# Optimization experiments

Hardware: AMD Instinct MI355X
Metric: run time of the kernel (lower is better)

Reference implementation:

```python
import jax, jax.numpy as jnp
import numpy as np

B, LIN, LOUT = 16, 100, 100
V, D, AD, H, HID = 32000, 512, 64, 8, 2048
RECYCLE, PAD = 1, 0
SCALE = float(np.sqrt(AD))

def _pe(L, dim):
    # positional(pos, i) = pos / 10000 ** ((i//2)/dim); sin on even i, cos on odd i
    pos = jnp.arange(L, dtype=jnp.float32)[:, None]
    i = jnp.arange(dim)
    ang = pos / jnp.power(jnp.float32(10000.0), (i // 2).astype(jnp.float32) / dim)
    return jnp.where(i % 2 == 0, jnp.sin(ang), jnp.cos(ang))  # (L, dim)

def _ln(x, g, b):
    m = x.mean(-1, keepdims=True)
    v = ((x - m) ** 2).mean(-1, keepdims=True)
    return (x - m) / jnp.sqrt(v + 1e-5) * g + b

def _mha(q, k, v, mask, p):
    wq, bq, wk, bk, wv, bv, wo, bo, g, b = p
    m, lq, _ = q.shape
    lk = k.shape[1]
    Q = (q @ wq + bq).reshape(m, lq, H, AD).transpose(0, 2, 1, 3)
    K = (k @ wk + bk).reshape(m, lk, H, AD).transpose(0, 2, 1, 3)
    Vh = (v @ wv + bv).reshape(m, lk, H, AD).transpose(0, 2, 1, 3)
    attn = jnp.einsum('mnld,mnkd->mnlk', Q / SCALE, K)
    attn = jnp.where(mask[:, None, :, :], attn, jnp.float32(-1e9))
    attn = jax.nn.softmax(attn, axis=-1)
    o = jnp.einsum('mnlk,mnkd->mnld', attn, Vh)
    # original uses rearrange 'm n l d -> m l (d n)': d is the OUTER factor
    o = o.transpose(0, 2, 3, 1).reshape(m, lq, AD * H)
    o = o @ wo + bo + q  # dropout is identity in eval
    return _ln(o, g, b)

def _ff(x, w1, b1, w2, b2, g, b):
    return _ln(jax.nn.relu(x @ w1 + b1) @ w2 + b2 + x, g, b)

def _forward(floats, inputs, outputs):
    (sw, fcb,
     ewq, ebq, ewk, ebk, ewv, ebv, ewo, ebo, eg1, eb1, ef1w, ef1b, ef2w, ef2b, eg2, eb2,
     dwq, dbq, dwk, dbk, dwv, dbv, dwo, dbo, dg1, db1, df1w, df1b, df2w, df2b, dg2, db2) = floats
    enc_p = (ewq, ebq, ewk, ebk, ewv, ebv, ewo, ebo, eg1, eb1)
    dec_p = (dwq, dbq, dwk, dbk, dwv, dbv, dwo, dbo, dg1, db1)
    in_mask = (inputs != PAD)[:, None, :]                    # (B,1,LIN) -> bcast (B,1,1,LIN)
    tril = jnp.tril(jnp.ones((LOUT, LOUT), dtype=bool))
    out_mask = (outputs != PAD)[:, None, :] & tril[None]     # (B,LOUT,LOUT)
    enc = sw[inputs] + _pe(LIN, D)[None]
    for _ in range(RECYCLE + 1):  # shared weights reused each iteration
        enc = _mha(enc, enc, enc, in_mask, enc_p)
        enc = _ff(enc, ef1w, ef1b, ef2w, ef2b, eg2, eb2)
    dec = sw[outputs] + _pe(LOUT, D)[None]
    for _ in range(RECYCLE + 1):  # same MHA module for self- and cross-attention
        dec = _mha(dec, dec, dec, out_mask, dec_p)
        dec = _mha(dec, enc, enc, in_mask, dec_p)
        dec = _ff(dec, df1w, df1b, df2w, df2b, dg2, db2)
    dec = dec * jnp.float32(D ** -0.5)
    logits = dec @ sw.T + fcb  # fc.weight tied to share_weight
    return jax.nn.softmax(logits, axis=-1)

def setup_inputs():
    key = jax.random.key(0)
    ks = iter(jax.random.split(key, 64))
    rn = lambda shape: jax.random.normal(next(ks), shape, dtype=jnp.float32) * 0.02
    z = lambda shape: jnp.zeros(shape, jnp.float32)
    o = lambda shape: jnp.ones(shape, jnp.float32)
    d = {'inputs': jax.random.randint(next(ks), (B, LIN), 0, V),
         'outputs': jax.random.randint(next(ks), (B, LOUT), 0, V),
         'share_weight': rn((V, D)), 'fc_b': z((V,))}
    for p in ('enc', 'dec'):
        d[f'{p}_wq'] = rn((D, H * AD)); d[f'{p}_bq'] = z((H * AD,))
        d[f'{p}_wk'] = rn((D, H * AD)); d[f'{p}_bk'] = z((H * AD,))
        d[f'{p}_wv'] = rn((D, H * AD)); d[f'{p}_bv'] = z((H * AD,))
        d[f'{p}_wo'] = rn((H * AD, D)); d[f'{p}_bo'] = z((D,))
        d[f'{p}_g1'] = o((D,)); d[f'{p}_b1'] = z((D,))
        d[f'{p}_f1w'] = rn((D, HID)); d[f'{p}_f1b'] = z((HID,))
        d[f'{p}_f2w'] = rn((HID, D)); d[f'{p}_f2b'] = z((D,))
        d[f'{p}_g2'] = o((D,)); d[f'{p}_b2'] = z((D,))
    return d

def reference(inputs, outputs, share_weight, fc_b, enc_wq, enc_bq, enc_wk, enc_bk, enc_wv, enc_bv, enc_wo, enc_bo, enc_g1, enc_b1, enc_f1w, enc_f1b, enc_f2w, enc_f2b, enc_g2, enc_b2, dec_wq, dec_bq, dec_wk, dec_bk, dec_wv, dec_bv, dec_wo, dec_bo, dec_g1, dec_b1, dec_f1w, dec_f1b, dec_f2w, dec_f2b, dec_g2, dec_b2):
    floats = (share_weight, fc_b, enc_wq, enc_bq, enc_wk, enc_bk, enc_wv, enc_bv, enc_wo, enc_bo, enc_g1, enc_b1, enc_f1w, enc_f1b, enc_f2w, enc_f2b, enc_g2, enc_b2, dec_wq, dec_bq, dec_wk, dec_bk, dec_wv, dec_bv, dec_wo, dec_bo, dec_g1, dec_b1, dec_f1w, dec_f1b, dec_f2w, dec_f2b, dec_g2, dec_b2)
    return _forward(floats, inputs, outputs)
```

## Files before the change

kernel.cpp:

```cpp
#include <hip/hip_runtime.h>

#define TQ     1600
#define MP     1664
#define DM     512
#define NHD    8
#define HD     64
#define VOCAB  32000
#define HID    2048
#define LSEQ   100
#define NSTRIPE 500
#define SCALEV 0.044194173824159216f

typedef unsigned short u16;
typedef unsigned int u32;
typedef __attribute__((ext_vector_type(8))) short bf16x8;
typedef __attribute__((ext_vector_type(4))) float f32x4;

__device__ __forceinline__ u16 f2b(float x) {
  union { float f; unsigned u; } c; c.f = x;
  unsigned r = (c.u + 0x7FFFu + ((c.u >> 16) & 1u)) >> 16;
  return (u16)r;
}
__device__ __forceinline__ float b2f(u16 b) {
  union { unsigned u; float f; } c; c.u = ((unsigned)b) << 16; return c.f;
}
__device__ __forceinline__ unsigned pk2(float lo, float hi) {
  return (unsigned)f2b(lo) | ((unsigned)f2b(hi) << 16);
}
__device__ __forceinline__ float wredsum(float v) {
#pragma unroll
  for (int o = 32; o > 0; o >>= 1) v += __shfl_xor(v, o, 64);
  return v;
}

struct PrepArgs {
  const float* wsrc[12];
  u16* wdst[12];
  int K[12], N[12], toff[12];
  int ntile;
  const float* bsrc[6];
  float* qbE; float* qbD; float* peT;
};

__global__ __launch_bounds__(256) void prep_kernel(PrepArgs a) {
  __shared__ float t[64][65];
  int bid = blockIdx.x, tid = threadIdx.x;
  if (bid < a.ntile) {
    int wi = 0;
#pragma unroll
    for (int i = 1; i < 12; ++i) if (bid >= a.toff[i]) wi = i;
    int tile = bid - a.toff[wi];
    int K = a.K[wi], N = a.N[wi];
    int ktiles = K >> 6;
    int k0 = (tile % ktiles) << 6, n0 = (tile / ktiles) << 6;
    const float* src = a.wsrc[wi];
    u16* dst = a.wdst[wi];
    int r = tid >> 4, c = (tid & 15) * 4;
#pragma unroll
    for (int i = 0; i < 4; ++i) {
      float4 v = *(const float4*)(src + (size_t)(k0 + r + i * 16) * N + n0 + c);
      t[r + i * 16][c + 0] = v.x; t[r + i * 16][c + 1] = v.y;
      t[r + i * 16][c + 2] = v.z; t[r + i * 16][c + 3] = v.w;
    }
    __syncthreads();
#pragma unroll
    for (int i = 0; i < 4; ++i) {
      int n = r + i * 16;
      ushort4 o;
      o.x = f2b(t[c + 0][n]); o.y = f2b(t[c + 1][n]);
      o.z = f2b(t[c + 2][n]); o.w = f2b(t[c + 3][n]);
      *(ushort4*)(dst + (size_t)(n0 + n) * K + k0 + c) = o;
    }
  } else if (bid < a.ntile + 12) {
    int j = (bid - a.ntile) * 256 + tid;
    if (j < 3072) {
      int which = j >> 9, o = j & 511;
      float v = a.bsrc[which][o];
      if (which < 3) a.qbE[which * 512 + o] = v;
      else           a.qbD[(which - 3) * 512 + o] = v;
    }
  } else {
    int idx = (bid - a.ntile - 12) * 256 + tid;
    if (idx < LSEQ * 512) {
      int l = idx >> 9, d = idx & 511;
      float freq = expf(-(float)(d >> 1) * (9.210340371976184f / 512.0f));
      float ang = (float)l * freq;
      a.peT[idx] = (d & 1) ? cosf(ang) : sinf(ang);
    }
  }
}

__global__ __launch_bounds__(256) void embed_kernel(const int* __restrict__ tokA,
                                                    const int* __restrict__ tokB,
                                                    const float* __restrict__ sw,
                                                    const float* __restrict__ peT,
                                                    u16* __restrict__ bufA,
                                                    u16* __restrict__ bufB) {
  const int half = MP * DM / 256;
  int bid = blockIdx.x;
  const int* tok = (bid < half) ? tokA : tokB;
  u16* out = (bid < half) ? bufA : bufB;
  int idx = (bid < half ? bid : bid - half) * 256 + threadIdx.x;
  int row = idx >> 9, d = idx & 511;
  float v = 0.f;
  if (row < TQ) {
    int l = row % LSEQ;
    int t = tok[row];
    v = sw[(size_t)t * DM + d] + peT[l * 512 + d];
  }
  out[idx] = f2b(v);
}

template<bool RELU, bool RES>
__global__ __launch_bounds__(256) void bgemm_kernel(
    const u16* __restrict__ A, const u16* __restrict__ BT,
    const float* __restrict__ bias, const u16* __restrict__ res,
    u16* __restrict__ C, int K, int ldc)
{
  __shared__ u16 As[64 * 64];
  __shared__ u16 Bs[64 * 64];
  const int tid = threadIdx.x;
  const int m0 = blockIdx.y << 6, n0 = blockIdx.x << 6;
  const int w = tid >> 6, lane = tid & 63;
  const int c = lane & 15, q = lane >> 4;
  const int tr = tid >> 3, tc = tid & 7;
  const int sbase = tr * 128 + ((tc * 16) ^ ((tr & 7) << 4));
  const u16* agp = A + (size_t)(m0 + tr) * K + tc * 8;
  const u16* bgp = BT + (size_t)(n0 + tr) * K + tc * 8;
  const int arow = w * 16 + c;
  f32x4 acc[4];
#pragma unroll
  for (int t = 0; t < 4; ++t) acc[t] = (f32x4){0.f, 0.f, 0.f, 0.f};

  for (int k0 = 0; k0 < K; k0 += 64) {
    __syncthreads();
#pragma unroll
    for (int rep = 0; rep < 2; ++rep) {
      uint4 va = *(const uint4*)(agp + k0 + (size_t)rep * 32 * K);
      uint4 vb = *(const uint4*)(bgp + k0 + (size_t)rep * 32 * K);
      *(uint4*)((char*)As + sbase + rep * 4096) = va;
      *(uint4*)((char*)Bs + sbase + rep * 4096) = vb;
    }
    __syncthreads();
#pragma unroll
    for (int ks = 0; ks < 2; ++ks) {
      bf16x8 af = *(bf16x8*)((char*)As + arow * 128 + ((ks * 64 + q * 16) ^ ((arow & 7) << 4)));
#pragma unroll
      for (int t = 0; t < 4; ++t) {
        int brow = t * 16 + c;
        bf16x8 bf = *(bf16x8*)((char*)Bs + brow * 128 + ((ks * 64 + q * 16) ^ ((brow & 7) << 4)));
        acc[t] = __builtin_amdgcn_mfma_f32_16x16x32_bf16(af, bf, acc[t], 0, 0, 0);
      }
    }
  }
#pragma unroll
  for (int t = 0; t < 4; ++t) {
    int col = n0 + t * 16 + c;
    float bsv = bias[col];
#pragma unroll
    for (int r = 0; r < 4; ++r) {
      int row = m0 + w * 16 + q * 4 + r;
      float v = acc[t][r] + bsv;
      if (RES) v += b2f(res[(size_t)row * ldc + col]);
      if (RELU) v = fmaxf(v, 0.f);
      C[(size_t)row * ldc + col] = f2b(v);
    }
  }
}

__global__ __launch_bounds__(256) void ln_kernel(u16* __restrict__ X,
                                                 const float* __restrict__ g,
                                                 const float* __restrict__ b) {
  int row = blockIdx.x * 4 + (threadIdx.x >> 6);
  int lane = threadIdx.x & 63;
  u16* p = X + (size_t)row * DM + lane * 8;
  uint4 u = *(uint4*)p;
  unsigned uu[4] = {u.x, u.y, u.z, u.w};
  float x[8];
#pragma unroll
  for (int e = 0; e < 4; ++e) {
    x[e * 2]     = b2f((u16)(uu[e] & 0xffff));
    x[e * 2 + 1] = b2f((u16)(uu[e] >> 16));
  }
  float s = 0.f;
#pragma unroll
  for (int j = 0; j < 8; ++j) s += x[j];
  s = wredsum(s);
  float mean = s * (1.0f / 512.0f);
  float d2 = 0.f;
#pragma unroll
  for (int j = 0; j < 8; ++j) { float d = x[j] - mean; d2 += d * d; }
  d2 = wredsum(d2);
  float r = rsqrtf(d2 * (1.0f / 512.0f) + 1e-5f);
  const float* gg = g + lane * 8;
  const float* bb = b + lane * 8;
  float y[8];
#pragma unroll
  for (int j = 0; j < 8; ++j) y[j] = (x[j] - mean) * r * gg[j] + bb[j];
  uint4 o;
  o.x = pk2(y[0], y[1]); o.y = pk2(y[2], y[3]);
  o.z = pk2(y[4], y[5]); o.w = pk2(y[6], y[7]);
  *(uint4*)p = o;
}

__global__ __launch_bounds__(256) void attn_kernel(
    const u16* __restrict__ QKV, const int* __restrict__ tok,
    u16* __restrict__ O, int causal)
{
  __shared__ u16 Qs[64 * 64];
  __shared__ u16 Ks[112 * 64];
  __shared__ u16 Vt[64 * 128];
  __shared__ u16 Ps[64 * 128];
  __shared__ int tokv[112];
  int bid = blockIdx.x;
  int b = bid >> 4, h = (bid >> 1) & 7, half = bid & 1;
  int tid = threadIdx.x;

  for (int i = tid; i < 4096; i += 256) ((u32*)Vt)[i] = 0;
  for (int i = tid; i < 4096; i += 256) ((u32*)Ps)[i] = 0;
  if (tid < 112) tokv[tid] = (tid < 100) ? (tok[b * LSEQ + tid] != 0) : 0;
  __syncthreads();

  const size_t rowbase = (size_t)(b * LSEQ) * 1536 + h * 64;
  for (int i = tid; i < 896; i += 256) {
    int r = i >> 3, c8 = i & 7;
    size_t g = rowbase + (size_t)r * 1536 + c8 * 8;
    int off = (c8 * 16) ^ ((r & 7) << 4);
    uint4 k4 = *(const uint4*)(QKV + g + 512);
    *(uint4*)((char*)Ks + r * 128 + off) = k4;
    if (r < 64) {
      uint4 q4 = *(const uint4*)(QKV + g + (size_t)(half * 64) * 1536);
      *(uint4*)((char*)Qs + r * 128 + off) = q4;
    }
    if (r < LSEQ) {
      union { uint4 u; u16 s[8]; } cv;
      cv.u = *(const uint4*)(QKV + g + 1024);
#pragma unroll
      for (int j = 0; j < 8; ++j) {
        int d = c8 * 8 + j;
        *(u16*)((char*)Vt + d * 256 + ((2 * r) ^ ((d & 7) << 4))) = cv.s[j];
      }
    }
  }
  __syncthreads();

  const int lane = tid & 63, w = tid >> 6;
  const int c = lane & 15, q = lane >> 4;
  const int mt = w;
  const int mbase = half * 64 + mt * 16;
  if (mbase < 112) {
    f32x4 s[7];
#pragma unroll
    for (int nt = 0; nt < 7; ++nt) s[nt] = (f32x4){0.f, 0.f, 0.f, 0.f};
    int arow = mt * 16 + c;
    int axr = (arow & 7) << 4;
    bf16x8 a0 = *(bf16x8*)((char*)Qs + arow * 128 + ((q * 16) ^ axr));
    bf16x8 a1 = *(bf16x8*)((char*)Qs + arow * 128 + ((64 + q * 16) ^ axr));
#pragma unroll
    for (int nt = 0; nt < 7; ++nt) {
      int brow = nt * 16 + c;
      int bxr = (brow & 7) << 4;
      bf16x8 b0 = *(bf16x8*)((char*)Ks + brow * 128 + ((q * 16) ^ bxr));
      bf16x8 b1 = *(bf16x8*)((char*)Ks + brow * 128 + ((64 + q * 16) ^ bxr));
      s[nt] = __builtin_amdgcn_mfma_f32_16x16x32_bf16(a0, b0, s[nt], 0, 0, 0);
      s[nt] = __builtin_amdgcn_mfma_f32_16x16x32_bf16(a1, b1, s[nt], 0, 0, 0);
    }
#pragma unroll
    for (int r = 0; r < 4; ++r) {
      int mrow = mbase + q * 4 + r;
      int ml = mt * 16 + q * 4 + r;
      float sv[7];
      float mx = -3.0e38f;
#pragma unroll
      for (int nt = 0; nt < 7; ++nt) {
        int kcol = nt * 16 + c;
        float x = s[nt][r];
        bool real = kcol < LSEQ;
        bool ok = real && tokv[kcol] && (!causal || kcol <= mrow);
        x = ok ? x * 0.125f : (real ? -1e9f : -3.0e38f);
        sv[nt] = x;
        mx = fmaxf(mx, x);
      }
#pragma unroll
      for (int o = 1; o < 16; o <<= 1) mx = fmaxf(mx, __shfl_xor(mx, o, 64));
      float sum = 0.f;
#pragma unroll
      for (int nt = 0; nt < 7; ++nt) { sv[nt] = __expf(sv[nt] - mx); sum += sv[nt]; }
#pragma unroll
      for (int o = 1; o < 16; o <<= 1) sum += __shfl_xor(sum, o, 64);
      float inv = 1.0f / sum;
      int pxr = (ml & 7) << 4;
#pragma unroll
      for (int nt = 0; nt < 7; ++nt) {
        int kcol = nt * 16 + c;
        *(u16*)((char*)Ps + ml * 256 + ((2 * kcol) ^ pxr)) = f2b(sv[nt] * inv);
      }
    }
    asm volatile("s_waitcnt lgkmcnt(0)" ::: "memory");
    __builtin_amdgcn_sched_barrier(0);
    int prow = mt * 16 + c;
    int pxr2 = (prow & 7) << 4;
    bf16x8 pa[4];
#pragma unroll
    for (int ks = 0; ks < 4; ++ks)
      pa[ks] = *(bf16x8*)((char*)Ps + prow * 256 + ((ks * 64 + q * 16) ^ pxr2));
#pragma unroll
    for (int dt = 0; dt < 4; ++dt) {
      f32x4 o = (f32x4){0.f, 0.f, 0.f, 0.f};
      int vrow = dt * 16 + c;
      int vxr = (vrow & 7) << 4;
#pragma unroll
      for (int ks = 0; ks < 4; ++ks) {
        bf16x8 vb = *(bf16x8*)((char*)Vt + vrow * 256 + ((ks * 64 + q * 16) ^ vxr));
        o = __builtin_amdgcn_mfma_f32_16x16x32_bf16(pa[ks], vb, o, 0, 0, 0);
      }
#pragma unroll
      for (int r = 0; r < 4; ++r) {
        int mrow = mbase + q * 4 + r;
        if (mrow < LSEQ) {
          int d = dt * 16 + c;
          O[(size_t)(b * LSEQ + mrow) * DM + d * 8 + h] = f2b(o[r]);
        }
      }
    }
  }
}

template<bool PART>
__global__ __launch_bounds__(512) void vgemm_kernel(
    const u16* __restrict__ A, const float* __restrict__ sw,
    const float* __restrict__ fcb, float* __restrict__ out,
    float2* __restrict__ pbuf)
{
  __shared__ u16 Bs[8][64 * 64];
  const int tid = threadIdx.x;
  const int n0 = blockIdx.x << 6;
  for (int i = tid; i < 4096; i += 512) {
    int row = i >> 6, uk = i & 63;
    const float* s = sw + (size_t)(n0 + row) * DM + uk * 8;
    float4 f0 = *(const float4*)s;
    float4 f1 = *(const float4*)(s + 4);
    uint4 o;
    o.x = pk2(f0.x, f0.y); o.y = pk2(f0.z, f0.w);
    o.z = pk2(f1.x, f1.y); o.w = pk2(f1.z, f1.w);
    *(uint4*)((char*)Bs + (uk >> 3) * 8192 + row * 128 +
              (((uk & 7) * 16) ^ ((row & 7) << 4))) = o;
  }
  __syncthreads();

  const int lane = tid & 63, w = tid >> 6;
  const int c = lane & 15, q = lane >> 4;
  float fb[4];
#pragma unroll
  for (int ni = 0; ni < 4; ++ni) fb[ni] = fcb[n0 + ni * 16 + c];

  for (int mt = w; mt < 25; mt += 8) {
    const int rowbase = mt * 64;
    f32x4 acc[4][4];
#pragma unroll
    for (int mi = 0; mi < 4; ++mi)
#pragma unroll
      for (int ni = 0; ni < 4; ++ni) acc[mi][ni] = (f32x4){0.f, 0.f, 0.f, 0.f};
    const u16* pA[4];
#pragma unroll
    for (int mi = 0; mi < 4; ++mi)
      pA[mi] = A + (size_t)(rowbase + mi * 16 + c) * DM + q * 8;
#pragma unroll 2
    for (int ks = 0; ks < 16; ++ks) {
      bf16x8 af[4], bf[4];
#pragma unroll
      for (int mi = 0; mi < 4; ++mi) {
        union { uint4 u; bf16x8 b; } ca;
        ca.u = *(const uint4*)(pA[mi] + ks * 32);
        af[mi] = ca.b;
      }
#pragma unroll
      for (int ni = 0; ni < 4; ++ni) {
        int brow = ni * 16 + c;
        bf[ni] = *(bf16x8*)((char*)Bs + (ks >> 1) * 8192 + brow * 128 +
                            ((((ks & 1) * 64) + q * 16) ^ ((brow & 7) << 4)));
      }
#pragma unroll
      for (int mi = 0; mi < 4; ++mi)
#pragma unroll
        for (int ni = 0; ni < 4; ++ni)
          acc[mi][ni] = __builtin_amdgcn_mfma_f32_16x16x32_bf16(af[mi], bf[ni], acc[mi][ni], 0, 0, 0);
    }
#pragma unroll
    for (int mi = 0; mi < 4; ++mi) {
      int row0 = rowbase + mi * 16 + q * 4;
      float lv[4][4];
#pragma unroll
      for (int ni = 0; ni < 4; ++ni)
#pragma unroll
        for (int r = 0; r < 4; ++r) lv[ni][r] = acc[mi][ni][r] * SCALEV + fb[ni];
#pragma unroll
      for (int ni = 0; ni < 4; ++ni) {
        int col = n0 + ni * 16 + c;
#pragma unroll
        for (int r = 0; r < 4; ++r)
          out[(size_t)(row0 + r) * VOCAB + col] = lv[ni][r];
      }
      if (PART) {
        float pm[4], ps[4];
#pragma unroll
        for (int r = 0; r < 4; ++r) {
          float mx = fmaxf(fmaxf(lv[0][r], lv[1][r]), fmaxf(lv[2][r], lv[3][r]));
#pragma unroll
          for (int o = 1; o < 16; o <<= 1) mx = fmaxf(mx, __shfl_xor(mx, o, 64));
          float ss = __expf(lv[0][r] - mx) + __expf(lv[1][r] - mx) +
                     __expf(lv[2][r] - mx) + __expf(lv[3][r] - mx);
#pragma unroll
          for (int o = 1; o < 16; o <<= 1) ss += __shfl_xor(ss, o, 64);
          pm[r] = mx; ps[r] = ss;
        }
        if (c < 4)
          pbuf[(size_t)(row0 + c) * NSTRIPE + blockIdx.x] = make_float2(pm[c], ps[c]);
      }
    }
  }
}

__global__ __launch_bounds__(256) void reduce_partials(const float2* __restrict__ pbuf,
                                                       float2* __restrict__ MS) {
  int row = blockIdx.x * 4 + (threadIdx.x >> 6);
  int lane = threadIdx.x & 63;
  float m = -3.0e38f, s = 0.f;
  for (int i = lane; i < NSTRIPE; i += 64) {
    float2 p = pbuf[(size_t)row * NSTRIPE + i];
    float mn = fmaxf(m, p.x);
    s = s * __expf(m - mn) + p.y * __expf(p.x - mn);
    m = mn;
  }
#pragma unroll
  for (int o = 1; o < 64; o <<= 1) {
    float m2 = __shfl_xor(m, o, 64);
    float s2 = __shfl_xor(s, o, 64);
    float mn = fmaxf(m, m2);
    s = s * __expf(m - mn) + s2 * __expf(m2 - mn);
    m = mn;
  }
  if (lane == 0) MS[row] = make_float2(m, 1.0f / s);
}

__global__ __launch_bounds__(256) void rowstat_kernel(const float* __restrict__ L,
                                                      float2* __restrict__ MS) {
  __shared__ float am[4], as_[4];
  int row = blockIdx.x, tid = threadIdx.x;
  const float* p = L + (size_t)row * VOCAB;
  float m = -3.0e38f, s = 0.f;
  for (int i = tid; i < VOCAB; i += 256) {
    float x = p[i];
    if (x > m) { s *= __expf(m - x); m = x; }
    s += __expf(x - m);
  }
#pragma unroll
  for (int o = 1; o < 64; o <<= 1) {
    float m2 = __shfl_xor(m, o, 64);
    float s2 = __shfl_xor(s, o, 64);
    float mn = fmaxf(m, m2);
    s = s * __expf(m - mn) + s2 * __expf(m2 - mn);
    m = mn;
  }
  if ((tid & 63) == 0) { am[tid >> 6] = m; as_[tid >> 6] = s; }
  __syncthreads();
  if (tid == 0) {
    float M = am[0], S = as_[0];
#pragma unroll
    for (int k = 1; k < 4; ++k) {
      float mn = fmaxf(M, am[k]);
      S = S * __expf(M - mn) + as_[k] * __expf(am[k] - mn);
      M = mn;
    }
    MS[row] = make_float2(M, 1.0f / S);
  }
}

__global__ __launch_bounds__(256) void vfinal_kernel(float* __restrict__ P,
                                                     const float2* __restrict__ MS) {
  int row = blockIdx.y;
  int col = blockIdx.x * 1024 + threadIdx.x * 4;
  if (col >= VOCAB) return;
  float2 ms = MS[row];
  float* p = P + (size_t)row * VOCAB + col;
  float4 x = *(float4*)p;
  x.x = __expf(x.x - ms.x) * ms.y;
  x.y = __expf(x.y - ms.x) * ms.y;
  x.z = __expf(x.z - ms.x) * ms.y;
  x.w = __expf(x.w - ms.x) * ms.y;
  *(float4*)p = x;
}

extern "C" void kernel_launch(void* const* d_in, const int* in_sizes, int n_in,
                              void* d_out, int out_size, void* d_ws, size_t ws_size,
                              hipStream_t stream) {
  (void)in_sizes; (void)n_in; (void)out_size;
  const int* inputs  = (const int*)d_in[0];
  const int* outputs = (const int*)d_in[1];
  const float* sw  = (const float*)d_in[2];
  const float* fcb = (const float*)d_in[3];
  const float* E[16];
  const float* Dd[16];
  for (int i = 0; i < 16; ++i) E[i]  = (const float*)d_in[4 + i];
  for (int i = 0; i < 16; ++i) Dd[i] = (const float*)d_in[20 + i];

  u16* bufE = (u16*)d_ws;
  u16* bufD = bufE + (size_t)MP * DM;
  size_t offMS = (size_t)2 * MP * DM * 2;
  size_t offPB = offMS + (size_t)TQ * 8;
  size_t need  = offPB + (size_t)TQ * NSTRIPE * 8;
  float2* MS   = (float2*)((char*)d_ws + offMS);
  float2* pbuf = (float2*)((char*)d_ws + offPB);
  bool part = ws_size >= need;

  char* base = (char*)d_out;
  size_t off = 0;
  auto carve = [&](size_t bytes) { void* p = base + off; off += (bytes + 255) & ~(size_t)255; return p; };
  u16* bqkvE = (u16*)carve((size_t)MP * 1536 * 2);
  u16* bqkvD = (u16*)carve((size_t)MP * 1536 * 2);
  u16* ba    = (u16*)carve((size_t)MP * DM * 2);
  u16* bh    = (u16*)carve((size_t)MP * HID * 2);
  u16* wqkvE = (u16*)carve((size_t)1536 * 512 * 2);
  u16* woE   = (u16*)carve((size_t)512 * 512 * 2);
  u16* f1E   = (u16*)carve((size_t)2048 * 512 * 2);
  u16* f2E   = (u16*)carve((size_t)512 * 2048 * 2);
  u16* wqkvD = (u16*)carve((size_t)1536 * 512 * 2);
  u16* woD   = (u16*)carve((size_t)512 * 512 * 2);
  u16* f1D   = (u16*)carve((size_t)2048 * 512 * 2);
  u16* f2D   = (u16*)carve((size_t)512 * 2048 * 2);
  float* qbE = (float*)carve(1536 * 4);
  float* qbD = (float*)carve(1536 * 4);
  float* peT = (float*)carve((size_t)LSEQ * 512 * 4);
  float* out = (float*)d_out;

  PrepArgs pa;
  const float* ws_[12] = {E[0], E[2], E[4], E[6], E[10], E[12],
                          Dd[0], Dd[2], Dd[4], Dd[6], Dd[10], Dd[12]};
  u16* wd_[12] = {wqkvE, wqkvE + 512 * 512, wqkvE + 1024 * 512, woE, f1E, f2E,
                  wqkvD, wqkvD + 512 * 512, wqkvD + 1024 * 512, woD, f1D, f2D};
  int K_[12] = {512, 512, 512, 512, 512, 2048, 512, 512, 512, 512, 512, 2048};
  int N_[12] = {512, 512, 512, 512, 2048, 512, 512, 512, 512, 512, 2048, 512};
  int tiles = 0;
  for (int i = 0; i < 12; ++i) {
    pa.wsrc[i] = ws_[i]; pa.wdst[i] = wd_[i]; pa.K[i] = K_[i]; pa.N[i] = N_[i];
    pa.toff[i] = tiles;
    tiles += (K_[i] >> 6) * (N_[i] >> 6);
  }
  pa.ntile = tiles;
  const float* bs_[6] = {E[1], E[3], E[5], Dd[1], Dd[3], Dd[5]};
  for (int i = 0; i < 6; ++i) pa.bsrc[i] = bs_[i];
  pa.qbE = qbE; pa.qbD = qbD; pa.peT = peT;
  prep_kernel<<<tiles + 12 + 200, 256, 0, stream>>>(pa);

  embed_kernel<<<2 * MP * DM / 256, 256, 0, stream>>>(inputs, outputs, sw, peT, bufE, bufD);

  const dim3 Gqkv(24, 26), G512(8, 26), Gkv(16, 26), Ghid(32, 26);

  for (int it = 0; it < 2; ++it) {
    bgemm_kernel<false,false><<<Gqkv,256,0,stream>>>(bufE, wqkvE, qbE, nullptr, bqkvE, 512, 1536);
    attn_kernel<<<256,256,0,stream>>>(bqkvE, inputs, ba, 0);
    bgemm_kernel<false,true><<<G512,256,0,stream>>>(ba, woE, E[7], bufE, bufE, 512, 512);
    ln_kernel<<<TQ/4,256,0,stream>>>(bufE, E[8], E[9]);
    bgemm_kernel<true,false><<<Ghid,256,0,stream>>>(bufE, f1E, E[11], nullptr, bh, 512, 2048);
    bgemm_kernel<false,true><<<G512,256,0,stream>>>(bh, f2E, E[13], bufE, bufE, 2048, 512);
    ln_kernel<<<TQ/4,256,0,stream>>>(bufE, E[14], E[15]);
  }
  bgemm_kernel<false,false><<<Gkv,256,0,stream>>>(bufE, wqkvD + 512 * 512, qbD + 512, nullptr, bqkvD + 512, 512, 1536);
  for (int it = 0; it < 2; ++it) {
    bgemm_kernel<false,false><<<Gqkv,256,0,stream>>>(bufD, wqkvD, qbD, nullptr, bqkvE, 512, 1536);
    attn_kernel<<<256,256,0,stream>>>(bqkvE, outputs, ba, 1);
    bgemm_kernel<false,true><<<G512,256,0,stream>>>(ba, woD, Dd[7], bufD, bufD, 512, 512);
    ln_kernel<<<TQ/4,256,0,stream>>>(bufD, Dd[8], Dd[9]);
    bgemm_kernel<false,false><<<G512,256,0,stream>>>(bufD, wqkvD, qbD, nullptr, bqkvD, 512, 1536);
    attn_kernel<<<256,256,0,stream>>>(bqkvD, inputs, ba, 0);
    bgemm_kernel<false,true><<<G512,256,0,stream>>>(ba, woD, Dd[7], bufD, bufD, 512, 512);
    ln_kernel<<<TQ/4,256,0,stream>>>(bufD, Dd[8], Dd[9]);
    bgemm_kernel<true,false><<<Ghid,256,0,stream>>>(bufD, f1D, Dd[11], nullptr, bh, 512, 2048);
    bgemm_kernel<false,true><<<G512,256,0,stream>>>(bh, f2D, Dd[13], bufD, bufD, 2048, 512);
    ln_kernel<<<TQ/4,256,0,stream>>>(bufD, Dd[14], Dd[15]);
  }

  if (part) {
    vgemm_kernel<true><<<NSTRIPE, 512, 0, stream>>>(bufD, sw, fcb, out, pbuf);
    reduce_partials<<<TQ / 4, 256, 0, stream>>>(pbuf, MS);
  } else {
    vgemm_kernel<false><<<NSTRIPE, 512, 0, stream>>>(bufD, sw, fcb, out, nullptr);
    rowstat_kernel<<<TQ, 256, 0, stream>>>(out, MS);
  }
  vfinal_kernel<<<dim3(32, TQ), 256, 0, stream>>>(out, MS);
}
```

Measured before the change: 649.9 us.

## Recompute vocab GEMM to fuse softmax normalization and skip logits round-trip

The vocab projection now runs twice. The first pass only produces per-stripe max/sum partials and writes no logits. After the partials are reduced, a second pass recomputes the logits and writes the normalized softmax directly. This removes one full write and read-modify-write of the 1600x32000 fp32 output in exchange for redoing the GEMM. It also double-buffers the A-operand global loads across k-steps, so the next k-step's loads overlap the MFMAs of the current one.

New measurement: 917.5 us. 41.2% more time.

```diff
diff --git a/kernel.cpp b/kernel.cpp
--- a/kernel.cpp
+++ b/kernel.cpp
@@ -326,11 +326,11 @@
   }
 }
 
-template<bool PART>
+template<int MODE>
 __global__ __launch_bounds__(512) void vgemm_kernel(
     const u16* __restrict__ A, const float* __restrict__ sw,
     const float* __restrict__ fcb, float* __restrict__ out,
-    float2* __restrict__ pbuf)
+    float2* __restrict__ pbuf, const float2* __restrict__ MS)
 {
   __shared__ u16 Bs[8][64 * 64];
   const int tid = threadIdx.x;
@@ -365,26 +365,38 @@
 #pragma unroll
     for (int mi = 0; mi < 4; ++mi)
       pA[mi] = A + (size_t)(rowbase + mi * 16 + c) * DM + q * 8;
-#pragma unroll 2
+
+    uint4 ap[2][4];
+#pragma unroll
+    for (int mi = 0; mi < 4; ++mi) ap[0][mi] = *(const uint4*)(pA[mi]);
+#pragma unroll
+    for (int mi = 0; mi < 4; ++mi) ap[1][mi] = *(const uint4*)(pA[mi] + 32);
+
+#pragma unroll
     for (int ks = 0; ks < 16; ++ks) {
-      bf16x8 af[4], bf[4];
-#pragma unroll
-      for (int mi = 0; mi < 4; ++mi) {
-        union { uint4 u; bf16x8 b; } ca;
-        ca.u = *(const uint4*)(pA[mi] + ks * 32);
-        af[mi] = ca.b;
-      }
+      bf16x8 bf[4];
 #pragma unroll
       for (int ni = 0; ni < 4; ++ni) {
         int brow = ni * 16 + c;
         bf[ni] = *(bf16x8*)((char*)Bs + (ks >> 1) * 8192 + brow * 128 +
                             ((((ks & 1) * 64) + q * 16) ^ ((brow & 7) << 4)));
       }
+      bf16x8 af[4];
+#pragma unroll
+      for (int mi = 0; mi < 4; ++mi) {
+        union { uint4 u; bf16x8 b; } cv; cv.u = ap[ks & 1][mi];
+        af[mi] = cv.b;
+      }
 #pragma unroll
       for (int mi = 0; mi < 4; ++mi)
 #pragma unroll
         for (int ni = 0; ni < 4; ++ni)
           acc[mi][ni] = __builtin_amdgcn_mfma_f32_16x16x32_bf16(af[mi], bf[ni], acc[mi][ni], 0, 0, 0);
+      if (ks < 14) {
+#pragma unroll
+        for (int mi = 0; mi < 4; ++mi)
+          ap[ks & 1][mi] = *(const uint4*)(pA[mi] + (ks + 2) * 32);
+      }
     }
 #pragma unroll
     for (int mi = 0; mi < 4; ++mi) {
@@ -394,14 +406,7 @@
       for (int ni = 0; ni < 4; ++ni)
 #pragma unroll
         for (int r = 0; r < 4; ++r) lv[ni][r] = acc[mi][ni][r] * SCALEV + fb[ni];
-#pragma unroll
-      for (int ni = 0; ni < 4; ++ni) {
-        int col = n0 + ni * 16 + c;
-#pragma unroll
-        for (int r = 0; r < 4; ++r)
-          out[(size_t)(row0 + r) * VOCAB + col] = lv[ni][r];
-      }
-      if (PART) {
+      if (MODE == 0) {
         float pm[4], ps[4];
 #pragma unroll
         for (int r = 0; r < 4; ++r) {
@@ -416,6 +421,25 @@
         }
         if (c < 4)
           pbuf[(size_t)(row0 + c) * NSTRIPE + blockIdx.x] = make_float2(pm[c], ps[c]);
+      } else if (MODE == 1) {
+        float2 msv[4];
+#pragma unroll
+        for (int r = 0; r < 4; ++r) msv[r] = MS[row0 + r];
+#pragma unroll
+        for (int ni = 0; ni < 4; ++ni) {
+          int col = n0 + ni * 16 + c;
+#pragma unroll
+          for (int r = 0; r < 4; ++r)
+            out[(size_t)(row0 + r) * VOCAB + col] = __expf(lv[ni][r] - msv[r].x) * msv[r].y;
+        }
+      } else {
+#pragma unroll
+        for (int ni = 0; ni < 4; ++ni) {
+          int col = n0 + ni * 16 + c;
+#pragma unroll
+          for (int r = 0; r < 4; ++r)
+            out[(size_t)(row0 + r) * VOCAB + col] = lv[ni][r];
+        }
       }
     }
   }
@@ -581,11 +605,12 @@
   }
 
   if (part) {
-    vgemm_kernel<true><<<NSTRIPE, 512, 0, stream>>>(bufD, sw, fcb, out, pbuf);
+    vgemm_kernel<0><<<NSTRIPE, 512, 0, stream>>>(bufD, sw, fcb, nullptr, pbuf, nullptr);
     reduce_partials<<<TQ / 4, 256, 0, stream>>>(pbuf, MS);
+    vgemm_kernel<1><<<NSTRIPE, 512, 0, stream>>>(bufD, sw, fcb, out, nullptr, MS);
   } else {
-    vgemm_kernel<false><<<NSTRIPE, 512, 0, stream>>>(bufD, sw, fcb, out, nullptr);
+    vgemm_kernel<2><<<NSTRIPE, 512, 0, stream>>>(bufD, sw, fcb, out, nullptr, nullptr);
     rowstat_kernel<<<TQ, 256, 0, stream>>>(out, MS);
-  }
-  vfinal_kernel<<<dim3(32, TQ), 256, 0, stream>>>(out, MS);
-}
+    vfinal_kernel<<<dim3(32, TQ), 256, 0, stream>>>(out, MS);
+  }
+}
```

## Recompute vocab GEMM to fuse softmax normalization, avoiding logits write and reread

Applied to the files above, without the earlier changes.

The vocab projection now runs twice. The first pass only produces per-row max/sum partials with no logits store, then the partials are reduced, and a second pass recomputes the GEMM and writes normalized softmax outputs directly. This removes the full 1600x32000 fp32 logit write, its reread and rewrite in the final softmax kernel, at the cost of doing the GEMM twice. The MFMA operands are also swapped so each lane holds 4 consecutive columns, which allows float4 stores and a simpler row reduction.

Result: slower. 681.5 us (+4.9%).

```diff
diff --git a/kernel.cpp b/kernel.cpp
--- a/kernel.cpp
+++ b/kernel.cpp
@@ -326,11 +326,11 @@
   }
 }
 
-template<bool PART>
+template<int MODE>
 __global__ __launch_bounds__(512) void vgemm_kernel(
     const u16* __restrict__ A, const float* __restrict__ sw,
     const float* __restrict__ fcb, float* __restrict__ out,
-    float2* __restrict__ pbuf)
+    float2* __restrict__ pbuf, const float2* __restrict__ MS)
 {
   __shared__ u16 Bs[8][64 * 64];
   const int tid = threadIdx.x;
@@ -350,72 +350,87 @@
 
   const int lane = tid & 63, w = tid >> 6;
   const int c = lane & 15, q = lane >> 4;
-  float fb[4];
-#pragma unroll
-  for (int ni = 0; ni < 4; ++ni) fb[ni] = fcb[n0 + ni * 16 + c];
+  float4 fb[4];
+#pragma unroll
+  for (int ni = 0; ni < 4; ++ni)
+    fb[ni] = *(const float4*)(fcb + n0 + ni * 16 + q * 4);
 
   for (int mt = w; mt < 25; mt += 8) {
     const int rowbase = mt * 64;
     f32x4 acc[4][4];
 #pragma unroll
+    for (int ni = 0; ni < 4; ++ni)
+#pragma unroll
+      for (int mi = 0; mi < 4; ++mi) acc[ni][mi] = (f32x4){0.f, 0.f, 0.f, 0.f};
+    const u16* pB[4];
+#pragma unroll
     for (int mi = 0; mi < 4; ++mi)
-#pragma unroll
-      for (int ni = 0; ni < 4; ++ni) acc[mi][ni] = (f32x4){0.f, 0.f, 0.f, 0.f};
-    const u16* pA[4];
-#pragma unroll
-    for (int mi = 0; mi < 4; ++mi)
-      pA[mi] = A + (size_t)(rowbase + mi * 16 + c) * DM + q * 8;
+      pB[mi] = A + (size_t)(rowbase + mi * 16 + c) * DM + q * 8;
 #pragma unroll 2
     for (int ks = 0; ks < 16; ++ks) {
-      bf16x8 af[4], bf[4];
-#pragma unroll
-      for (int mi = 0; mi < 4; ++mi) {
-        union { uint4 u; bf16x8 b; } ca;
-        ca.u = *(const uint4*)(pA[mi] + ks * 32);
-        af[mi] = ca.b;
-      }
+      bf16x8 sf[4], bfr[4];
 #pragma unroll
       for (int ni = 0; ni < 4; ++ni) {
         int brow = ni * 16 + c;
-        bf[ni] = *(bf16x8*)((char*)Bs + (ks >> 1) * 8192 + brow * 128 +
+        sf[ni] = *(bf16x8*)((char*)Bs + (ks >> 1) * 8192 + brow * 128 +
                             ((((ks & 1) * 64) + q * 16) ^ ((brow & 7) << 4)));
       }
 #pragma unroll
-      for (int mi = 0; mi < 4; ++mi)
+      for (int mi = 0; mi < 4; ++mi) {
+        union { uint4 u; bf16x8 b; } cv;
+        cv.u = *(const uint4*)(pB[mi] + ks * 32);
+        bfr[mi] = cv.b;
+      }
+#pragma unroll
+      for (int ni = 0; ni < 4; ++ni)
+#pragma unroll
+        for (int mi = 0; mi < 4; ++mi)
+          acc[ni][mi] = __builtin_amdgcn_mfma_f32_16x16x32_bf16(sf[ni], bfr[mi], acc[ni][mi], 0, 0, 0);
+    }
+#pragma unroll
+    for (int mi = 0; mi < 4; ++mi) {
+      int m = rowbase + mi * 16 + c;
+      float lv[4][4];
+#pragma unroll
+      for (int ni = 0; ni < 4; ++ni) {
+        const float* fbp = (const float*)&fb[ni];
+#pragma unroll
+        for (int r = 0; r < 4; ++r) lv[ni][r] = acc[ni][mi][r] * SCALEV + fbp[r];
+      }
+      if (MODE == 0) {
+        float mx = -3.0e38f;
 #pragma unroll
         for (int ni = 0; ni < 4; ++ni)
-          acc[mi][ni] = __builtin_amdgcn_mfma_f32_16x16x32_bf16(af[mi], bf[ni], acc[mi][ni], 0, 0, 0);
-    }
-#pragma unroll
-    for (int mi = 0; mi < 4; ++mi) {
-      int row0 = rowbase + mi * 16 + q * 4;
-      float lv[4][4];
-#pragma unroll
-      for (int ni = 0; ni < 4; ++ni)
-#pragma unroll
-        for (int r = 0; r < 4; ++r) lv[ni][r] = acc[mi][ni][r] * SCALEV + fb[ni];
-#pragma unroll
-      for (int ni = 0; ni < 4; ++ni) {
-        int col = n0 + ni * 16 + c;
-#pragma unroll
-        for (int r = 0; r < 4; ++r)
-          out[(size_t)(row0 + r) * VOCAB + col] = lv[ni][r];
-      }
-      if (PART) {
-        float pm[4], ps[4];
-#pragma unroll
-        for (int r = 0; r < 4; ++r) {
-          float mx = fmaxf(fmaxf(lv[0][r], lv[1][r]), fmaxf(lv[2][r], lv[3][r]));
-#pragma unroll
-          for (int o = 1; o < 16; o <<= 1) mx = fmaxf(mx, __shfl_xor(mx, o, 64));
-          float ss = __expf(lv[0][r] - mx) + __expf(lv[1][r] - mx) +
-                     __expf(lv[2][r] - mx) + __expf(lv[3][r] - mx);
-#pragma unroll
-          for (int o = 1; o < 16; o <<= 1) ss += __shfl_xor(ss, o, 64);
-          pm[r] = mx; ps[r] = ss;
+#pragma unroll
+          for (int r = 0; r < 4; ++r) mx = fmaxf(mx, lv[ni][r]);
+        mx = fmaxf(mx, __shfl_xor(mx, 16, 64));
+        mx = fmaxf(mx, __shfl_xor(mx, 32, 64));
+        float ss = 0.f;
+#pragma unroll
+        for (int ni = 0; ni < 4; ++ni)
+#pragma unroll
+          for (int r = 0; r < 4; ++r) ss += __expf(lv[ni][r] - mx);
+        ss += __shfl_xor(ss, 16, 64);
+        ss += __shfl_xor(ss, 32, 64);
+        if (q == 0)
+          pbuf[(size_t)m * NSTRIPE + blockIdx.x] = make_float2(mx, ss);
+      } else if (MODE == 1) {
+        float2 msv = MS[m];
+#pragma unroll
+        for (int ni = 0; ni < 4; ++ni) {
+          float4 o4;
+          o4.x = __expf(lv[ni][0] - msv.x) * msv.y;
+          o4.y = __expf(lv[ni][1] - msv.x) * msv.y;
+          o4.z = __expf(lv[ni][2] - msv.x) * msv.y;
+          o4.w = __expf(lv[ni][3] - msv.x) * msv.y;
+          *(float4*)(out + (size_t)m * VOCAB + n0 + ni * 16 + q * 4) = o4;
         }
-        if (c < 4)
-          pbuf[(size_t)(row0 + c) * NSTRIPE + blockIdx.x] = make_float2(pm[c], ps[c]);
+      } else {
+#pragma unroll
+        for (int ni = 0; ni < 4; ++ni) {
+          float4 o4 = make_float4(lv[ni][0], lv[ni][1], lv[ni][2], lv[ni][3]);
+          *(float4*)(out + (size_t)m * VOCAB + n0 + ni * 16 + q * 4) = o4;
+        }
       }
     }
   }
@@ -581,11 +596,12 @@
   }
 
   if (part) {
-    vgemm_kernel<true><<<NSTRIPE, 512, 0, stream>>>(bufD, sw, fcb, out, pbuf);
+    vgemm_kernel<0><<<NSTRIPE, 512, 0, stream>>>(bufD, sw, fcb, nullptr, pbuf, nullptr);
     reduce_partials<<<TQ / 4, 256, 0, stream>>>(pbuf, MS);
+    vgemm_kernel<1><<<NSTRIPE, 512, 0, stream>>>(bufD, sw, fcb, out, nullptr, MS);
   } else {
-    vgemm_kernel<false><<<NSTRIPE, 512, 0, stream>>>(bufD, sw, fcb, out, nullptr);
+    vgemm_kernel<2><<<NSTRIPE, 512, 0, stream>>>(bufD, sw, fcb, out, nullptr, nullptr);
     rowstat_kernel<<<TQ, 256, 0, stream>>>(out, MS);
-  }
-  vfinal_kernel<<<dim3(32, TQ), 256, 0, stream>>>(out, MS);
-}
+    vfinal_kernel<<<dim3(32, TQ), 256, 0, stream>>>(out, MS);
+  }
+}
```
